# Kernel optimization log

Hardware: AMD Instinct MI355X
Metric: run time of the kernel (lower is better)

Reference implementation:

```python
import jax, jax.numpy as jnp
import numpy as np

D_MODEL = 1024
NUM_HEADS = 16
DEPTH = D_MODEL // NUM_HEADS


def setup_inputs() -> dict:
    key = jax.random.key(0)
    ks = jax.random.split(key, 10)
    B, LQ, LK = 4, 2048, 2048
    # xavier_uniform bound for square [d,d] weight
    bound = float(np.sqrt(6.0 / (D_MODEL + D_MODEL)))
    def w(k):
        return jax.random.uniform(k, (D_MODEL, D_MODEL), jnp.float32, -bound, bound)
    return {
        "query": jax.random.normal(ks[0], (B, LQ, D_MODEL), jnp.float32),
        "value": jax.random.normal(ks[1], (B, LK, D_MODEL), jnp.float32),
        "wq": w(ks[2]), "bq": jnp.zeros((D_MODEL,), jnp.float32),
        "wk": w(ks[3]), "bk": jnp.zeros((D_MODEL,), jnp.float32),
        "wv": w(ks[4]), "bv": jnp.zeros((D_MODEL,), jnp.float32),
        "wo": w(ks[5]), "bo": jnp.zeros((D_MODEL,), jnp.float32),
    }


def _split_heads(x, B):
    # [B, L, d_model] -> [B, H, L, depth]
    return x.reshape(B, -1, NUM_HEADS, DEPTH).transpose(0, 2, 1, 3)


def reference(query, value, wq, bq, wk, bk, wv, bv, wo, bo):
    B = query.shape[0]
    # torch nn.Linear: y = x @ W.T + b
    q = _split_heads(query @ wq.T + bq, B)          # [B,H,Lq,depth]
    k = _split_heads(value @ wk.T + bk, B)          # [B,H,Lk,depth]
    v = _split_heads(value @ wv.T + bv, B)          # [B,H,Lk,depth]
    scale = jnp.sqrt(jnp.asarray(DEPTH, dtype=q.dtype))
    scores = jnp.einsum("bhqd,bhkd->bhqk", q, k) / scale
    attn = jax.nn.softmax(scores, axis=-1)
    ctx = jnp.einsum("bhqk,bhkd->bhqd", attn, v)    # [B,H,Lq,depth]
    ctx = ctx.transpose(0, 2, 1, 3).reshape(B, -1, D_MODEL)
    return ctx @ wo.T + bo
```

## Files before the change

### kernel.cpp

```cpp
#include <hip/hip_runtime.h>
#include <hip/hip_bf16.h>

typedef unsigned short u16;
typedef unsigned int u32;
typedef __attribute__((ext_vector_type(8))) short bf16x8;
typedef __attribute__((ext_vector_type(4))) float f32x4;

#define MFMA16(a, b, c) __builtin_amdgcn_mfma_f32_16x16x32_bf16(a, b, c, 0, 0, 0)

#define QSCALE 0.18033688011112042f

__device__ inline u16 f2b(float f) {
    union { float f; unsigned int i; } v;
    v.f = f;
    unsigned int r = v.i + 0x7fffu + ((v.i >> 16) & 1u);
    return (u16)(r >> 16);
}
__device__ inline u32 fbits(float f) {
    union { float f; u32 i; } v; v.f = f; return v.i;
}
__device__ inline u32 pack2_trunc(float f0, float f1) {
    return __builtin_amdgcn_perm(fbits(f1), fbits(f0), 0x07060302u);
}

__device__ inline void glds16(const u16* g, u16* l) {
    __builtin_amdgcn_global_load_lds(
        (const __attribute__((address_space(1))) unsigned int*)g,
        (__attribute__((address_space(3))) unsigned int*)l, 16, 0, 0);
}

__global__ __launch_bounds__(256) void cvt_all(
    const float* __restrict__ q, const float* __restrict__ v,
    const float* __restrict__ wq, const float* __restrict__ wk,
    const float* __restrict__ wv, const float* __restrict__ wo,
    u16* __restrict__ qb, u16* __restrict__ vb,
    u16* __restrict__ wqb, u16* __restrict__ wkb,
    u16* __restrict__ wvb, u16* __restrict__ wob)
{
    int flat = blockIdx.x;
    const float* x; u16* y; int off;
    if (flat < 8192) {
        x = flat < 4096 ? q : v;
        y = flat < 4096 ? qb : vb;
        off = flat & 4095;
    } else {
        int s = (flat - 8192) >> 9;
        off = (flat - 8192) & 511;
        x = s == 0 ? wq : (s == 1 ? wk : (s == 2 ? wv : wo));
        y = s == 0 ? wqb : (s == 1 ? wkb : (s == 2 ? wvb : wob));
    }
    int i = (off * 256 + threadIdx.x) * 8;
    float4 a = *(const float4*)(x + i);
    float4 b = *(const float4*)(x + i + 4);
    u16 o[8] = { f2b(a.x), f2b(a.y), f2b(a.z), f2b(a.w),
                 f2b(b.x), f2b(b.y), f2b(b.z), f2b(b.w) };
    *(uint4*)(y + i) = *(uint4*)o;
}

__global__ __launch_bounds__(256, 2) void gemm_proj(
    const u16* __restrict__ qb, const u16* __restrict__ vb,
    const u16* __restrict__ wqb, const u16* __restrict__ wkb,
    const u16* __restrict__ wvb,
    const float* __restrict__ bq, const float* __restrict__ bk,
    const float* __restrict__ bv,
    u16* __restrict__ Qp, u16* __restrict__ Kp, u16* __restrict__ VT,
    int M, int K)
{
    const int flat = blockIdx.x;
    const int xcd = flat & 7, idx = flat >> 3;
    const int mt  = xcd * 4 + (idx & 3);
    const int yy  = idx >> 2;
    const int sel = yy >> 3;
    const int n0 = (yy & 7) * 128;
    const u16* A = sel ? vb : qb;
    const u16* W = sel == 0 ? wqb : (sel == 1 ? wkb : wvb);
    const float* bias = sel == 0 ? bq : (sel == 1 ? bk : bv);
    const float cscale = sel == 0 ? QSCALE : 1.0f;

    __shared__ __align__(16) u16 As[256 * 64];
    __shared__ __align__(16) u16 Bs[128 * 64];

    const int tid  = threadIdx.x;
    const int wave = tid >> 6, lane = tid & 63;
    const int quad = lane >> 4, l16 = lane & 15;
    const int m0 = mt * 256;
    const int wm = (wave >> 1) * 128, wn = (wave & 1) * 64;

    f32x4 acc[8][4] = {};

    for (int k0 = 0; k0 < K; k0 += 64) {
        __syncthreads();
#pragma unroll
        for (int i = 0; i < 8; ++i) {
            int ch = tid + i * 256;
            int row = ch >> 3, c = ch & 7;
            glds16(&A[(size_t)(m0 + row) * K + k0 + ((c ^ (row & 7)) * 8)],
                   &As[ch * 8]);
        }
#pragma unroll
        for (int i = 0; i < 4; ++i) {
            int ch = tid + i * 256;
            int row = ch >> 3, c = ch & 7;
            glds16(&W[(size_t)(n0 + row) * K + k0 + ((c ^ (row & 7)) * 8)],
                   &Bs[ch * 8]);
        }
        __syncthreads();

#pragma unroll
        for (int ks = 0; ks < 2; ++ks) {
            bf16x8 af[8], bfr[4];
#pragma unroll
            for (int mi = 0; mi < 8; ++mi) {
                int row = wm + mi * 16 + l16;
                af[mi] = *(const bf16x8*)(
                    &As[row * 64 + (((ks * 4 + quad) ^ (row & 7)) * 8)]);
            }
#pragma unroll
            for (int ni = 0; ni < 4; ++ni) {
                int row = wn + ni * 16 + l16;
                bfr[ni] = *(const bf16x8*)(
                    &Bs[row * 64 + (((ks * 4 + quad) ^ (row & 7)) * 8)]);
            }
#pragma unroll
            for (int mi = 0; mi < 8; ++mi)
#pragma unroll
                for (int ni = 0; ni < 4; ++ni)
                    acc[mi][ni] = MFMA16(af[mi], bfr[ni], acc[mi][ni]);
        }
    }

    if (sel == 2) {
#pragma unroll
        for (int mi = 0; mi < 8; ++mi) {
#pragma unroll
            for (int ni = 0; ni < 4; ++ni) {
                int col = n0 + wn + ni * 16 + l16;
                float bv2 = bias[col];
                int row0 = m0 + wm + mi * 16 + quad * 4;
                int bb = row0 >> 11, l0 = row0 & 2047;
                u16 o[4];
#pragma unroll
                for (int r = 0; r < 4; ++r) o[r] = f2b(acc[mi][ni][r] + bv2);
                *(uint2*)(&VT[((size_t)bb * 1024 + col) * 2048 + l0]) = *(uint2*)o;
            }
        }
    } else {
        u16* C = sel == 0 ? Qp : Kp;
#pragma unroll
        for (int mi = 0; mi < 8; ++mi) {
#pragma unroll
            for (int ni = 0; ni < 4; ++ni) {
                int col = n0 + wn + ni * 16 + l16;
                float bv2 = bias[col];
#pragma unroll
                for (int r = 0; r < 4; ++r) {
                    int row = m0 + wm + mi * 16 + quad * 4 + r;
                    C[(size_t)row * 1024 + col] = f2b((acc[mi][ni][r] + bv2) * cscale);
                }
            }
        }
    }
}

__global__ __launch_bounds__(256) void gemm_out(
    const u16* __restrict__ A, const u16* __restrict__ B,
    const float* __restrict__ bias, float* __restrict__ C,
    int M, int N, int K)
{
    __shared__ __align__(16) u16 As[128 * 64];
    __shared__ __align__(16) u16 Bs[128 * 64];

    const int flat = blockIdx.x;
    const int xcd = flat & 7, idx = flat >> 3;
    const int mt  = xcd * 8 + (idx & 7);
    const int m0 = mt * 128, n0 = (idx >> 3) * 128;

    const int tid  = threadIdx.x;
    const int wave = tid >> 6, lane = tid & 63;
    const int quad = lane >> 4, l16 = lane & 15;
    const int wm = (wave >> 1) * 64, wn = (wave & 1) * 64;

    f32x4 acc[4][4] = {};

    for (int k0 = 0; k0 < K; k0 += 64) {
        __syncthreads();
#pragma unroll
        for (int i = 0; i < 4; ++i) {
            int ch = tid + i * 256;
            int row = ch >> 3, c = ch & 7;
            glds16(&A[(size_t)(m0 + row) * K + k0 + ((c ^ (row & 7)) * 8)],
                   &As[ch * 8]);
        }
#pragma unroll
        for (int i = 0; i < 4; ++i) {
            int ch = tid + i * 256;
            int row = ch >> 3, c = ch & 7;
            glds16(&B[(size_t)(n0 + row) * K + k0 + ((c ^ (row & 7)) * 8)],
                   &Bs[ch * 8]);
        }
        __syncthreads();

#pragma unroll
        for (int ks = 0; ks < 2; ++ks) {
            bf16x8 af[4], bfr[4];
#pragma unroll
            for (int mi = 0; mi < 4; ++mi) {
                int row = wm + mi * 16 + l16;
                af[mi] = *(const bf16x8*)(
                    &As[row * 64 + (((ks * 4 + quad) ^ (row & 7)) * 8)]);
            }
#pragma unroll
            for (int ni = 0; ni < 4; ++ni) {
                int row = wn + ni * 16 + l16;
                bfr[ni] = *(const bf16x8*)(
                    &Bs[row * 64 + (((ks * 4 + quad) ^ (row & 7)) * 8)]);
            }
#pragma unroll
            for (int mi = 0; mi < 4; ++mi)
#pragma unroll
                for (int ni = 0; ni < 4; ++ni)
                    acc[mi][ni] = MFMA16(af[mi], bfr[ni], acc[mi][ni]);
        }
    }

#pragma unroll
    for (int mi = 0; mi < 4; ++mi) {
#pragma unroll
        for (int ni = 0; ni < 4; ++ni) {
            int col = n0 + wn + ni * 16 + l16;
            float bv = bias[col];
#pragma unroll
            for (int r = 0; r < 4; ++r) {
                int row = m0 + wm + mi * 16 + quad * 4 + r;
                C[(size_t)row * N + col] = acc[mi][ni][r] + bv;
            }
        }
    }
}

__global__ __launch_bounds__(128, 2) void attn(
    const u16* __restrict__ Q, const u16* __restrict__ K,
    const u16* __restrict__ VT, u16* __restrict__ O,
    int LQ, int LK)
{
    const int tid  = threadIdx.x;
    const int wave = tid >> 6, lane = tid & 63;
    const int quad = lane >> 4, l16 = lane & 15;
    const int flat = blockIdx.x;
    const int xcd = flat & 7, slot = flat >> 3;
    const int bh = xcd * 8 + (slot >> 4);
    const int q0 = (slot & 15) * 128;
    const int b = bh >> 4, h = bh & 15;
    const size_t qbase = ((size_t)b * LQ + q0) * 1024 + h * 64;
    const size_t kbase = ((size_t)b * LK) * 1024 + h * 64;
    const size_t vtbase = ((size_t)b * 1024 + h * 64) * 2048;

    __shared__ __align__(16) u16 Ks[64 * 64];
    __shared__ __align__(16) u16 VTs[64 * 64];
    __shared__ __align__(16) u16 Ps[2][64 * 40];

    bf16x8 qf[4][2];
#pragma unroll
    for (int mi = 0; mi < 4; ++mi)
#pragma unroll
        for (int ks = 0; ks < 2; ++ks)
            qf[mi][ks] = *(const bf16x8*)(
                &Q[qbase + (size_t)(wave * 64 + mi * 16 + l16) * 1024 + ks * 32 + quad * 8]);

    const bf16x8 vones = { 0x3F80, 0x3F80, 0x3F80, 0x3F80,
                           0x3F80, 0x3F80, 0x3F80, 0x3F80 };

    f32x4 oacc[4][5] = {};

    const int swzr = (l16 & 7) << 3;

    for (int kt = 0; kt < LK; kt += 64) {
        __syncthreads();
#pragma unroll
        for (int i = 0; i < 4; ++i) {
            int ch = tid + i * 128;
            int row = ch >> 3;
            int csw = ((ch & 7) * 8) ^ ((row & 7) << 3);
            glds16(&K[kbase + (size_t)(kt + row) * 1024 + csw], &Ks[ch * 8]);
            glds16(&VT[vtbase + (size_t)row * 2048 + kt + csw], &VTs[ch * 8]);
        }
        __syncthreads();

        f32x4 st[4][4] = {};
#pragma unroll
        for (int ks = 0; ks < 2; ++ks) {
            bf16x8 kf[4];
#pragma unroll
            for (int ni = 0; ni < 4; ++ni)
                kf[ni] = *(const bf16x8*)(
                    &Ks[(ni * 16 + l16) * 64 + (((ks * 32) + quad * 8) ^ swzr)]);
            __builtin_amdgcn_s_setprio(1);
#pragma unroll
            for (int ni = 0; ni < 4; ++ni)
#pragma unroll
                for (int mi = 0; mi < 4; ++mi)
                    st[ni][mi] = MFMA16(kf[ni], qf[mi][ks], st[ni][mi]);
            __builtin_amdgcn_s_setprio(0);
        }

#pragma unroll
        for (int ks = 0; ks < 2; ++ks) {
#pragma unroll
            for (int mi = 0; mi < 4; ++mi)
#pragma unroll
                for (int ni2 = 0; ni2 < 2; ++ni2) {
                    const f32x4 s4 = st[ks * 2 + ni2][mi];
                    float p0 = __builtin_amdgcn_exp2f(s4[0]);
                    float p1 = __builtin_amdgcn_exp2f(s4[1]);
                    float p2 = __builtin_amdgcn_exp2f(s4[2]);
                    float p3 = __builtin_amdgcn_exp2f(s4[3]);
                    uint2 w;
                    w.x = pack2_trunc(p0, p1);
                    w.y = pack2_trunc(p2, p3);
                    *(uint2*)(&Ps[wave][(mi * 16 + l16) * 40 + ni2 * 16 + quad * 4]) = w;
                }

            bf16x8 vf[4];
#pragma unroll
            for (int nd = 0; nd < 4; ++nd)
                vf[nd] = *(const bf16x8*)(
                    &VTs[(nd * 16 + l16) * 64 + (((ks * 32) + quad * 8) ^ swzr)]);
            __builtin_amdgcn_s_setprio(1);
#pragma unroll
            for (int mi = 0; mi < 4; ++mi) {
                bf16x8 pf = *(const bf16x8*)(&Ps[wave][(mi * 16 + l16) * 40 + quad * 8]);
#pragma unroll
                for (int nd = 0; nd < 4; ++nd)
                    oacc[mi][nd] = MFMA16(pf, vf[nd], oacc[mi][nd]);
                oacc[mi][4] = MFMA16(pf, vones, oacc[mi][4]);
            }
            __builtin_amdgcn_s_setprio(0);
        }
    }

#pragma unroll
    for (int mi = 0; mi < 4; ++mi)
#pragma unroll
        for (int r = 0; r < 4; ++r) {
            float inv = 1.0f / oacc[mi][4][r];
            int row = q0 + wave * 64 + mi * 16 + quad * 4 + r;
            size_t rb = ((size_t)b * LQ + row) * 1024 + h * 64;
#pragma unroll
            for (int nd = 0; nd < 4; ++nd)
                O[rb + nd * 16 + l16] = f2b(oacc[mi][nd][r] * inv);
        }
}

extern "C" void kernel_launch(void* const* d_in, const int* in_sizes, int n_in,
                              void* d_out, int out_size, void* d_ws, size_t ws_size,
                              hipStream_t stream) {
    const float* query = (const float*)d_in[0];
    const float* value = (const float*)d_in[1];
    const float* wq = (const float*)d_in[2];
    const float* bq = (const float*)d_in[3];
    const float* wk = (const float*)d_in[4];
    const float* bk = (const float*)d_in[5];
    const float* wv = (const float*)d_in[6];
    const float* bv = (const float*)d_in[7];
    const float* wo = (const float*)d_in[8];
    const float* bo = (const float*)d_in[9];

    const int B = 4, LQ = 2048, LK = 2048, D = 1024;
    const int M = B * LQ;
    const int mat = M * D;
    const int wsz = D * D;

    u16* ws  = (u16*)d_ws;
    u16* qb  = ws;
    u16* vb  = qb + mat;
    u16* wqb = vb + mat;
    u16* wkb = wqb + wsz;
    u16* wvb = wkb + wsz;
    u16* wob = wvb + wsz;
    u16* Qp  = wob + wsz;
    u16* Kp  = Qp + mat;
    u16* Cp  = Kp + mat;
    u16* VT  = Cp + mat;

    dim3 blk(256);

    cvt_all<<<dim3(10240), blk, 0, stream>>>(
        query, value, wq, wk, wv, wo, qb, vb, wqb, wkb, wvb, wob);

    gemm_proj<<<dim3(768), blk, 0, stream>>>(
        qb, vb, wqb, wkb, wvb, bq, bk, bv, Qp, Kp, VT, M, D);

    attn<<<dim3(1024), dim3(128), 0, stream>>>(Qp, Kp, VT, Cp, LQ, LK);

    gemm_out<<<dim3(512), blk, 0, stream>>>(Cp, wob, bo, (float*)d_out, M, D, D);
}
```

Before: 299.1 us.

## Double-buffer LDS tiles in projection and output GEMMs to overlap loads

Both the fused QKV projection GEMM and the output GEMM now keep two LDS buffers and prefetch the next K-slice while MFMAs run on the current one, which cuts the per-iteration barriers from two to one. The QKV kernel also drops its K step from 64 to 32 and removes the XOR swizzle, using a plain 32-wide row layout. That layout may cause LDS bank conflicts, and the smaller K step means more loop iterations and barriers. The output GEMM doubles its LDS use, which may lower occupancy.

```diff
diff --git a/kernel.cpp b/kernel.cpp
--- a/kernel.cpp
+++ b/kernel.cpp
@@ -77,56 +77,60 @@
     const float* bias = sel == 0 ? bq : (sel == 1 ? bk : bv);
     const float cscale = sel == 0 ? QSCALE : 1.0f;
 
-    __shared__ __align__(16) u16 As[256 * 64];
-    __shared__ __align__(16) u16 Bs[128 * 64];
+    __shared__ __align__(16) u16 As[2][256 * 32];
+    __shared__ __align__(16) u16 Bs[2][128 * 32];
 
     const int tid  = threadIdx.x;
     const int wave = tid >> 6, lane = tid & 63;
     const int quad = lane >> 4, l16 = lane & 15;
     const int m0 = mt * 256;
     const int wm = (wave >> 1) * 128, wn = (wave & 1) * 64;
+    const int r0 = lane >> 2;
+    const int c0 = (lane & 3) * 8;
+    const int ra = wave * 16 + r0;
 
     f32x4 acc[8][4] = {};
 
-    for (int k0 = 0; k0 < K; k0 += 64) {
+    {
+#pragma unroll
+        for (int s = 0; s < 4; ++s)
+            glds16(&A[(size_t)(m0 + s * 64 + ra) * K + c0],
+                   &As[0][(s * 64 + ra) * 32 + c0]);
+#pragma unroll
+        for (int s = 0; s < 2; ++s)
+            glds16(&W[(size_t)(n0 + s * 64 + ra) * K + c0],
+                   &Bs[0][(s * 64 + ra) * 32 + c0]);
+    }
+    __syncthreads();
+
+    for (int k0 = 0; k0 < K; k0 += 32) {
+        const int cur = (k0 >> 5) & 1;
+        if (k0 + 32 < K) {
+            const int kn = k0 + 32;
+#pragma unroll
+            for (int s = 0; s < 4; ++s)
+                glds16(&A[(size_t)(m0 + s * 64 + ra) * K + kn + c0],
+                       &As[cur ^ 1][(s * 64 + ra) * 32 + c0]);
+#pragma unroll
+            for (int s = 0; s < 2; ++s)
+                glds16(&W[(size_t)(n0 + s * 64 + ra) * K + kn + c0],
+                       &Bs[cur ^ 1][(s * 64 + ra) * 32 + c0]);
+        }
+
+        bf16x8 af[8], bfr[4];
+#pragma unroll
+        for (int mi = 0; mi < 8; ++mi)
+            af[mi] = *(const bf16x8*)(&As[cur][(wm + mi * 16 + l16) * 32 + quad * 8]);
+#pragma unroll
+        for (int ni = 0; ni < 4; ++ni)
+            bfr[ni] = *(const bf16x8*)(&Bs[cur][(wn + ni * 16 + l16) * 32 + quad * 8]);
+#pragma unroll
+        for (int mi = 0; mi < 8; ++mi)
+#pragma unroll
+            for (int ni = 0; ni < 4; ++ni)
+                acc[mi][ni] = MFMA16(af[mi], bfr[ni], acc[mi][ni]);
+
         __syncthreads();
-#pragma unroll
-        for (int i = 0; i < 8; ++i) {
-            int ch = tid + i * 256;
-            int row = ch >> 3, c = ch & 7;
-            glds16(&A[(size_t)(m0 + row) * K + k0 + ((c ^ (row & 7)) * 8)],
-                   &As[ch * 8]);
-        }
-#pragma unroll
-        for (int i = 0; i < 4; ++i) {
-            int ch = tid + i * 256;
-            int row = ch >> 3, c = ch & 7;
-            glds16(&W[(size_t)(n0 + row) * K + k0 + ((c ^ (row & 7)) * 8)],
-                   &Bs[ch * 8]);
-        }
-        __syncthreads();
-
-#pragma unroll
-        for (int ks = 0; ks < 2; ++ks) {
-            bf16x8 af[8], bfr[4];
-#pragma unroll
-            for (int mi = 0; mi < 8; ++mi) {
-                int row = wm + mi * 16 + l16;
-                af[mi] = *(const bf16x8*)(
-                    &As[row * 64 + (((ks * 4 + quad) ^ (row & 7)) * 8)]);
-            }
-#pragma unroll
-            for (int ni = 0; ni < 4; ++ni) {
-                int row = wn + ni * 16 + l16;
-                bfr[ni] = *(const bf16x8*)(
-                    &Bs[row * 64 + (((ks * 4 + quad) ^ (row & 7)) * 8)]);
-            }
-#pragma unroll
-            for (int mi = 0; mi < 8; ++mi)
-#pragma unroll
-                for (int ni = 0; ni < 4; ++ni)
-                    acc[mi][ni] = MFMA16(af[mi], bfr[ni], acc[mi][ni]);
-        }
     }
 
     if (sel == 2) {
@@ -167,8 +171,8 @@
     const float* __restrict__ bias, float* __restrict__ C,
     int M, int N, int K)
 {
-    __shared__ __align__(16) u16 As[128 * 64];
-    __shared__ __align__(16) u16 Bs[128 * 64];
+    __shared__ __align__(16) u16 As[2][128 * 64];
+    __shared__ __align__(16) u16 Bs[2][128 * 64];
 
     const int flat = blockIdx.x;
     const int xcd = flat & 7, idx = flat >> 3;
@@ -182,23 +186,29 @@
 
     f32x4 acc[4][4] = {};
 
+#pragma unroll
+    for (int i = 0; i < 4; ++i) {
+        int ch = tid + i * 256;
+        int row = ch >> 3, c = ch & 7;
+        glds16(&A[(size_t)(m0 + row) * K + ((c ^ (row & 7)) * 8)], &As[0][ch * 8]);
+        glds16(&B[(size_t)(n0 + row) * K + ((c ^ (row & 7)) * 8)], &Bs[0][ch * 8]);
+    }
+    __syncthreads();
+
     for (int k0 = 0; k0 < K; k0 += 64) {
-        __syncthreads();
-#pragma unroll
-        for (int i = 0; i < 4; ++i) {
-            int ch = tid + i * 256;
-            int row = ch >> 3, c = ch & 7;
-            glds16(&A[(size_t)(m0 + row) * K + k0 + ((c ^ (row & 7)) * 8)],
-                   &As[ch * 8]);
-        }
-#pragma unroll
-        for (int i = 0; i < 4; ++i) {
-            int ch = tid + i * 256;
-            int row = ch >> 3, c = ch & 7;
-            glds16(&B[(size_t)(n0 + row) * K + k0 + ((c ^ (row & 7)) * 8)],
-                   &Bs[ch * 8]);
-        }
-        __syncthreads();
+        const int cur = (k0 >> 6) & 1;
+        if (k0 + 64 < K) {
+            const int kn = k0 + 64;
+#pragma unroll
+            for (int i = 0; i < 4; ++i) {
+                int ch = tid + i * 256;
+                int row = ch >> 3, c = ch & 7;
+                glds16(&A[(size_t)(m0 + row) * K + kn + ((c ^ (row & 7)) * 8)],
+                       &As[cur ^ 1][ch * 8]);
+                glds16(&B[(size_t)(n0 + row) * K + kn + ((c ^ (row & 7)) * 8)],
+                       &Bs[cur ^ 1][ch * 8]);
+            }
+        }
 
 #pragma unroll
         for (int ks = 0; ks < 2; ++ks) {
@@ -207,13 +217,13 @@
             for (int mi = 0; mi < 4; ++mi) {
                 int row = wm + mi * 16 + l16;
                 af[mi] = *(const bf16x8*)(
-                    &As[row * 64 + (((ks * 4 + quad) ^ (row & 7)) * 8)]);
+                    &As[cur][row * 64 + (((ks * 4 + quad) ^ (row & 7)) * 8)]);
             }
 #pragma unroll
             for (int ni = 0; ni < 4; ++ni) {
                 int row = wn + ni * 16 + l16;
                 bfr[ni] = *(const bf16x8*)(
-                    &Bs[row * 64 + (((ks * 4 + quad) ^ (row & 7)) * 8)]);
+                    &Bs[cur][row * 64 + (((ks * 4 + quad) ^ (row & 7)) * 8)]);
             }
 #pragma unroll
             for (int mi = 0; mi < 4; ++mi)
@@ -221,6 +231,8 @@
                 for (int ni = 0; ni < 4; ++ni)
                     acc[mi][ni] = MFMA16(af[mi], bfr[ni], acc[mi][ni]);
         }
+
+        __syncthreads();
     }
 
 #pragma unroll
```

Result: slower. 307.9 us (+2.9%).
